# Performance work log

Measured on AMD Instinct MI355X. Metric: run time of the kernel, lower is better.

Reference implementation:

```python
import jax, jax.numpy as jnp
import numpy as np

V_WORD, V_ENT, V_REL = 50000, 200000, 1000
B, S, CTX, T = 64, 128, 256, 10
E, D, H, C = 300, 100, 256, 3  # input_dim, triples_embedding_dim, hidden, classes
IN = E + 2 * D  # LSTM input size in graph_attention mode


def setup_inputs() -> dict:
    key = jax.random.key(0)
    ks = jax.random.split(key, 16)
    inputs = jax.random.randint(ks[0], (B, S), 0, V_WORD)
    context = jax.random.randint(ks[1], (B, CTX), 0, V_WORD)
    triples = jax.random.randint(ks[2], (B, S, T, 3), 0, V_REL)
    lengths = jax.random.randint(ks[3], (B,), 1, S + 1)  # valid lengths >= 1
    # id2_ids_batch: -1 sentinel means "no triple"; mix of -1 and valid
    id2_ids_batch = jax.random.randint(ks[4], (B, S, T), 0, 2) * 2 - 1
    embedding = jax.random.normal(ks[5], (V_WORD, E), jnp.float32) * 0.02
    embeddings_entity = jax.random.normal(ks[6], (V_ENT, D), jnp.float32) * 0.02
    embeddings_relation = jax.random.normal(ks[7], (V_REL, D), jnp.float32) * 0.02
    W_ent = jax.random.normal(ks[8], (D, 2 * D), jnp.float32) * 0.05  # entity_transformed (no bias)
    W_ih = jax.random.normal(ks[9], (4 * H, IN), jnp.float32) * 0.05
    W_hh = jax.random.normal(ks[10], (4 * H, H), jnp.float32) * 0.05
    b_lstm = jnp.zeros((4 * H,), jnp.float32)
    attn_w = jax.random.normal(ks[11], (1, H), jnp.float32) * 0.05
    attn_b = jnp.zeros((1,), jnp.float32)
    out_w = jax.random.normal(ks[12], (C, H), jnp.float32) * 0.05
    out_b = jnp.zeros((C,), jnp.float32)
    return dict(inputs=inputs, context=context, triples=triples, lengths=lengths,
                id2_ids_batch=id2_ids_batch, embedding=embedding,
                embeddings_entity=embeddings_entity, embeddings_relation=embeddings_relation,
                W_ent=W_ent, W_ih=W_ih, W_hh=W_hh, b_lstm=b_lstm,
                attn_w=attn_w, attn_b=attn_b, out_w=out_w, out_b=out_b)


def _lstm(x, W_ih, W_hh, b):
    """Single-layer unidirectional LSTM, PyTorch gate order (i,f,g,o). x: [B,S,I] -> [B,S,H]."""
    Hh = W_hh.shape[1]
    xg = jnp.einsum('bsi,gi->bsg', x, W_ih) + b  # precompute input projections [B,S,4H]
    def step(carry, xg_t):
        h, c = carry
        g = xg_t + h @ W_hh.T
        i, f, gg, o = jnp.split(g, 4, axis=-1)
        c = jax.nn.sigmoid(f) * c + jax.nn.sigmoid(i) * jnp.tanh(gg)
        h = jax.nn.sigmoid(o) * jnp.tanh(c)
        return (h, c), h
    h0 = jnp.zeros((x.shape[0], Hh), x.dtype)
    _, hs = jax.lax.scan(step, (h0, h0), jnp.swapaxes(xg, 0, 1))
    return jnp.swapaxes(hs, 0, 1)


def reference(inputs, context, triples, lengths, id2_ids_batch, embedding,
              embeddings_entity, embeddings_relation, W_ent, W_ih, W_hh, b_lstm,
              attn_w, attn_b, out_w, out_b):
    x = embedding[inputs]  # [B,S,E]
    # graph_attention branch, vectorized over (batch, token, triple)
    eh = embeddings_entity[triples[..., 0]]   # [B,S,T,D]
    et = embeddings_entity[triples[..., 1]]   # [B,S,T,D]
    er = embeddings_relation[triples[..., 2]] # [B,S,T,D]
    ht = jnp.concatenate([eh, et], axis=-1)   # [B,S,T,2D]
    tr = jnp.tanh(jnp.einsum('bstk,dk->bstd', ht, W_ent))  # entity_transformed + tanh
    e = jnp.sum(tr * er, axis=-1)             # [B,S,T]
    alpha = jax.nn.softmax(e, axis=-1)        # softmax over triples
    graph = jnp.einsum('bst,bstk->bsk', alpha, ht)  # [B,S,2D]
    valid = jnp.any(id2_ids_batch != -1, axis=-1)   # [B,S]; all -1 -> zeros (cc branch)
    graph = jnp.where(valid[..., None], graph, 0.0)
    t_in = jnp.concatenate([x, graph], axis=-1)     # [B,S,E+2D]
    out = _lstm(t_in, W_ih, W_hh, b_lstm)           # [B,S,H]
    # 'att' attention pooling, masked by lengths (pack/pad equivalent)
    mask = jnp.arange(S)[None, :] < lengths[:, None]
    scores = (jnp.einsum('bsh,oh->bso', out, attn_w) + attn_b)[..., 0]  # [B,S]
    a = jax.nn.softmax(jnp.where(mask, scores, -1e9), axis=-1)
    attended = jnp.einsum('bs,bsh->bh', a, out)     # [B,H]
    logits = attended @ out_w.T + out_b             # [B,C]
    return logits
```

## Files before the change

kernel.cpp:

```cpp
#include <hip/hip_runtime.h>
#include <cstdint>
#include <cstddef>

typedef unsigned int  uint_t;
typedef unsigned short ushort_t;

constexpr int B_  = 64;
constexpr int S_  = 128;
constexpr int D_  = 100;
constexpr int E_  = 300;
constexpr int H_  = 256;
constexpr int KIN = 512;
constexpr int NG  = 1024;
constexpr int M_  = B_ * S_;

constexpr size_t OFF_WT   = 0;
constexpr size_t OFF_FLAG = 40000;
constexpr size_t OFF_WIH  = 40960;
constexpr size_t OFF_WHH  = OFF_WIH + (size_t)NG * KIN * 2;
constexpr size_t OFF_TIN  = OFF_WHH + (size_t)128 * NG * 4;
constexpr size_t OFF_XG   = OFF_TIN + (size_t)M_ * KIN * 2;
constexpr size_t OFF_HOUT = OFF_XG + (size_t)M_ * NG * 4;

__device__ __forceinline__ float b2f(ushort_t u) {
  union { uint_t u; float f; } v; v.u = ((uint_t)u) << 16; return v.f;
}
__device__ __forceinline__ float blo(uint_t u) {
  union { uint_t u; float f; } v; v.u = u << 16; return v.f;
}
__device__ __forceinline__ float bhi(uint_t u) {
  union { uint_t u; float f; } v; v.u = u & 0xffff0000u; return v.f;
}
__device__ __forceinline__ ushort_t f2b(float f) {
  union { float f; uint_t u; } v; v.f = f;
  uint_t r = (v.u + 0x7fffu + ((v.u >> 16) & 1u)) >> 16;
  return (ushort_t)r;
}
__device__ __forceinline__ ushort_t f16bits(float f) {
  _Float16 h = (_Float16)f;
  union { _Float16 h; ushort_t u; } v; v.h = h; return v.u;
}
__device__ __forceinline__ uint_t pk16(float a, float b) {
  return (uint_t)f16bits(a) | ((uint_t)f16bits(b) << 16);
}
__device__ __forceinline__ float fast_tanh(float x) {
  float e = __expf(2.f * x);
  return 1.f - 2.f / (e + 1.f);
}
__device__ __forceinline__ float sigm(float x) {
  return 1.f / (1.f + __expf(-x));
}
__device__ __forceinline__ float ldv(const void* p, size_t i, int f32) {
  return f32 ? ((const float*)p)[i] : b2f(((const ushort_t*)p)[i]);
}

__device__ __forceinline__ float dot2(uint_t w, uint_t h, float acc) {
  union { uint_t u; _Float16 h[2]; } a, b; a.u = w; b.u = h;
  acc += (float)a.h[0] * (float)b.h[0];
  acc += (float)a.h[1] * (float)b.h[1];
  return acc;
}

__global__ __launch_bounds__(64) void k_detect(const uint_t* __restrict__ emb_w,
                                               char* __restrict__ ws)
{
  int tid = threadIdx.x;
  int hits = 0;
  for (int i = 0; i < 8; ++i) {
    uint_t w = emb_w[i * 64 + tid];
    uint_t e = (w >> 7) & 0xffu;
    hits += (e >= 140) ? 1 : 0;
  }
  for (int off = 32; off > 0; off >>= 1) hits += __shfl_down(hits, off);
  if (tid == 0) *(int*)(ws + OFF_FLAG) = (hits >= 32) ? 1 : 0;
}

__global__ __launch_bounds__(256) void k0_prep(
    const void* __restrict__ W_ent, const void* __restrict__ W_ih,
    const void* __restrict__ W_hh, char* __restrict__ ws)
{
  const int f32 = *(const int*)(ws + OFF_FLAG);
  int id = blockIdx.x * 256 + threadIdx.x;
  uint_t*   Wt = (uint_t*)(ws + OFF_WT);
  ushort_t* Wp = (ushort_t*)(ws + OFF_WIH);
  uint_t*   W2 = (uint_t*)(ws + OFF_WHH);
  if (id < 10000) {
    int kp = id / 100, d = id % 100;
    float a = ldv(W_ent, (size_t)d * 200 + 2 * kp,     f32);
    float b = ldv(W_ent, (size_t)d * 200 + 2 * kp + 1, f32);
    Wt[id] = pk16(a, b);
  } else if (id >= 20000 && id < 20000 + NG * KIN) {
    int i = id - 20000;
    int n = i >> 9, k = i & 511;
    Wp[i] = (k < 500) ? f2b(ldv(W_ih, (size_t)n * 500 + k, f32)) : (ushort_t)0;
  } else if (id >= 20000 + NG * KIN && id < 20000 + NG * KIN + 128 * NG) {
    int i = id - 20000 - NG * KIN;
    int row = i >> 7, kp = i & 127;
    float a = ldv(W_hh, (size_t)row * 256 + 2 * kp,     f32);
    float b = ldv(W_hh, (size_t)row * 256 + 2 * kp + 1, f32);
    W2[i] = pk16(a, b);
  }
}

__global__ __launch_bounds__(512) void k1_graph(
    const int* __restrict__ inputs, const int* __restrict__ triples,
    const int* __restrict__ id2, const void* __restrict__ emb,
    const void* __restrict__ ent, const void* __restrict__ rel,
    char* __restrict__ ws)
{
  __shared__ __align__(16) uint_t Wl2[10000];
  __shared__ uint_t htp[4][10][100];
  __shared__ float er_l[4][10][100];
  __shared__ float e_l[4][10];
  __shared__ float alpha_l[4][10];
  __shared__ int   trip_l[4][30];
  __shared__ int   vflag[4];

  const int tid = threadIdx.x;
  const int j   = tid >> 7;
  const int lt  = tid & 127;
  const int m   = blockIdx.x * 4 + j;
  const int f32 = *(const int*)(ws + OFF_FLAG);
  ushort_t* tin = (ushort_t*)(ws + OFF_TIN);

  if (lt < 30) trip_l[j][lt] = triples[(size_t)m * 30 + lt];
  if (lt == 0) vflag[j] = 0;
  if (lt < 10) e_l[j][lt] = 0.f;
  __syncthreads();
  if (lt < 10 && id2[(size_t)m * 10 + lt] != -1) atomicOr(&vflag[j], 1);

  {
    const uint4* src = (const uint4*)(ws + OFF_WT);
    uint4* dst = (uint4*)Wl2;
    for (int i = tid; i < 2500; i += 512) dst[i] = src[i];
  }
  for (int i = lt; i < 1000; i += 128) {
    int t = i / 100, kp = i % 100;
    int row = trip_l[j][t * 3 + (kp < 50 ? 0 : 1)];
    int off = (kp < 50) ? 2 * kp : 2 * (kp - 50);
    float x0, x1;
    if (f32) {
      float2 v = *(const float2*)((const float*)ent + (size_t)row * 100 + off);
      x0 = v.x; x1 = v.y;
    } else {
      uint_t u = *(const uint_t*)((const ushort_t*)ent + (size_t)row * 100 + off);
      x0 = blo(u); x1 = bhi(u);
    }
    htp[j][t][kp] = pk16(x0, x1);
  }
  for (int i = lt; i < 1000; i += 128) {
    int t = i / 100, d = i % 100;
    er_l[j][t][d] = ldv(rel, (size_t)trip_l[j][t * 3 + 2] * 100 + d, f32);
  }
  {
    int w = inputs[m];
    for (int c = lt; c < 300; c += 128)
      tin[(size_t)m * KIN + c] = f2b(ldv(emb, (size_t)w * E_ + c, f32));
    if (lt < 12) tin[(size_t)m * KIN + 500 + lt] = 0;
  }
  __syncthreads();

  if (lt < 125) {
    int t2 = lt / 25, d4 = lt % 25;
    int t0 = 2 * t2, t1 = t0 + 1;
    const uint_t* h0p = htp[j][t0];
    const uint_t* h1p = htp[j][t1];
    float a00 = 0, a01 = 0, a02 = 0, a03 = 0;
    float a10 = 0, a11 = 0, a12 = 0, a13 = 0;
    for (int kp = 0; kp < 100; ++kp) {
      uint4 wv = *(const uint4*)&Wl2[kp * 100 + 4 * d4];
      uint_t hp0 = h0p[kp], hp1 = h1p[kp];
      a00 = dot2(wv.x, hp0, a00); a01 = dot2(wv.y, hp0, a01);
      a02 = dot2(wv.z, hp0, a02); a03 = dot2(wv.w, hp0, a03);
      a10 = dot2(wv.x, hp1, a10); a11 = dot2(wv.y, hp1, a11);
      a12 = dot2(wv.z, hp1, a12); a13 = dot2(wv.w, hp1, a13);
    }
    int d = 4 * d4;
    float s0 = fast_tanh(a00) * er_l[j][t0][d]     + fast_tanh(a01) * er_l[j][t0][d + 1]
             + fast_tanh(a02) * er_l[j][t0][d + 2] + fast_tanh(a03) * er_l[j][t0][d + 3];
    float s1 = fast_tanh(a10) * er_l[j][t1][d]     + fast_tanh(a11) * er_l[j][t1][d + 1]
             + fast_tanh(a12) * er_l[j][t1][d + 2] + fast_tanh(a13) * er_l[j][t1][d + 3];
    atomicAdd(&e_l[j][t0], s0);
    atomicAdd(&e_l[j][t1], s1);
  }
  __syncthreads();
  if (lt == 0) {
    float mx = e_l[j][0];
    for (int t = 1; t < 10; ++t) mx = fmaxf(mx, e_l[j][t]);
    float s = 0.f;
    for (int t = 0; t < 10; ++t) { float v = __expf(e_l[j][t] - mx); alpha_l[j][t] = v; s += v; }
    float inv = 1.f / s;
    for (int t = 0; t < 10; ++t) alpha_l[j][t] *= inv;
  }
  __syncthreads();
  for (int kp = lt; kp < 100; kp += 128) {
    float g0 = 0.f, g1 = 0.f;
#pragma unroll
    for (int t = 0; t < 10; ++t) {
      union { uint_t u; _Float16 h[2]; } v; v.u = htp[j][t][kp];
      g0 += alpha_l[j][t] * (float)v.h[0];
      g1 += alpha_l[j][t] * (float)v.h[1];
    }
    if (!vflag[j]) { g0 = 0.f; g1 = 0.f; }
    tin[(size_t)m * KIN + 300 + 2 * kp]     = f2b(g0);
    tin[(size_t)m * KIN + 300 + 2 * kp + 1] = f2b(g1);
  }
}

typedef __attribute__((ext_vector_type(8))) short short8;
typedef __attribute__((ext_vector_type(4))) float f32x4;
typedef _Float16 half8 __attribute__((ext_vector_type(8)));

__global__ __launch_bounds__(256) void k2_xg(
    const void* __restrict__ bl, char* __restrict__ ws)
{
  __shared__ __align__(16) ushort_t As[128 * 32];
  __shared__ __align__(16) ushort_t Bs[128 * 32];
  const ushort_t* A  = (const ushort_t*)(ws + OFF_TIN);
  const ushort_t* Bw = (const ushort_t*)(ws + OFF_WIH);
  float* xg = (float*)(ws + OFF_XG);
  const int f32 = *(const int*)(ws + OFF_FLAG);

  const int tid = threadIdx.x;
  const int m0 = blockIdx.x * 128;
  const int n0 = blockIdx.y * 128;
  const int lane = tid & 63, wv = tid >> 6;
  const int wm = wv & 1, wn = wv >> 1;
  const int g = lane >> 4, r = lane & 15;

  f32x4 acc[4][4] = {};

  for (int ks = 0; ks < 16; ++ks) {
    const int k0 = ks * 32;
    {
      int c0 = tid, c1 = tid + 256;
      uint4 a0 = *(const uint4*)(A  + (size_t)(m0 + (c0 >> 2)) * KIN + k0 + ((c0 & 3) << 3));
      uint4 a1 = *(const uint4*)(A  + (size_t)(m0 + (c1 >> 2)) * KIN + k0 + ((c1 & 3) << 3));
      uint4 b0 = *(const uint4*)(Bw + (size_t)(n0 + (c0 >> 2)) * KIN + k0 + ((c0 & 3) << 3));
      uint4 b1 = *(const uint4*)(Bw + (size_t)(n0 + (c1 >> 2)) * KIN + k0 + ((c1 & 3) << 3));
      ((uint4*)As)[c0] = a0; ((uint4*)As)[c1] = a1;
      ((uint4*)Bs)[c0] = b0; ((uint4*)Bs)[c1] = b1;
    }
    __syncthreads();
    short8 av[4], bv[4];
#pragma unroll
    for (int i = 0; i < 4; ++i)
      av[i] = *(const short8*)&As[(wm * 64 + i * 16 + r) * 32 + g * 8];
#pragma unroll
    for (int j = 0; j < 4; ++j)
      bv[j] = *(const short8*)&Bs[(wn * 64 + j * 16 + r) * 32 + g * 8];
#pragma unroll
    for (int i = 0; i < 4; ++i)
#pragma unroll
      for (int j = 0; j < 4; ++j)
        acc[i][j] = __builtin_amdgcn_mfma_f32_16x16x32_bf16(av[i], bv[j], acc[i][j], 0, 0, 0);
    __syncthreads();
  }
#pragma unroll
  for (int j = 0; j < 4; ++j) {
    int n = n0 + wn * 64 + j * 16 + r;
    float bias = ldv(bl, n, f32);
#pragma unroll
    for (int i = 0; i < 4; ++i) {
      int mrow = m0 + wm * 64 + i * 16 + g * 4;
#pragma unroll
      for (int rr = 0; rr < 4; ++rr)
        xg[(size_t)(mrow + rr) * NG + n] = acc[i][j][rr] + bias;
    }
  }
}

__global__ __attribute__((amdgpu_waves_per_eu(2, 2))) __launch_bounds__(512)
void k3_lstm(char* __restrict__ ws)
{
  extern __shared__ __align__(16) char smem[];
  uint4*    ldsw = (uint4*)smem;
  float*    gbuf = (float*)(smem + 16 * 512 * 16);
  ushort_t* hbuf = (ushort_t*)(smem + 16 * 512 * 16 + 4096);

  const int tid = threadIdx.x;
  const int b   = blockIdx.x;
  const int w   = tid >> 6;
  const int l   = tid & 63;
  const int r   = l & 15;
  const int g   = l >> 4;
  const int rowbase = w * 128;

  const uint_t* W2 = (const uint_t*)(ws + OFF_WHH);
  const float* xg = (const float*)(ws + OFF_XG);
  float* hout = (float*)(ws + OFF_HOUT);

  uint4 wfrag[6][8];
#pragma unroll
  for (int mt = 0; mt < 6; ++mt)
#pragma unroll
    for (int kt = 0; kt < 8; ++kt)
      wfrag[mt][kt] = *(const uint4*)&W2[(size_t)(rowbase + mt * 16 + r) * 128 + kt * 16 + g * 4];
#pragma unroll
  for (int mt = 6; mt < 8; ++mt)
#pragma unroll
    for (int kt = 0; kt < 8; ++kt)
      ldsw[((mt - 6) * 8 + kt) * 512 + tid] =
        *(const uint4*)&W2[(size_t)(rowbase + mt * 16 + r) * 128 + kt * 16 + g * 4];

  hbuf[tid] = 0;
  float c = 0.f;
  const int bm = b * S_;
  float xn0 = 0.f, xn1 = 0.f, xn2 = 0.f, xn3 = 0.f;
  if (tid < 256) {
    const float* xp = xg + (size_t)bm * NG;
    xn0 = xp[tid]; xn1 = xp[tid + 256]; xn2 = xp[tid + 512]; xn3 = xp[tid + 768];
  }
  __syncthreads();

  for (int t = 0; t < S_; ++t) {
    const int cur = t & 1;
    const uint_t* hb = (const uint_t*)(hbuf + cur * 256);
#pragma unroll
    for (int hf = 0; hf < 2; ++hf) {
      f32x4 acc[4] = {};
#pragma unroll
      for (int kt = 0; kt < 8; ++kt) {
        union { uint4 u; half8 h; } bf;
        bf.u = make_uint4(0, 0, 0, 0);
        if (r == 0) bf.u = *(const uint4*)&hb[kt * 16 + g * 4];
#pragma unroll
        for (int m4 = 0; m4 < 4; ++m4) {
          const int mt = hf * 4 + m4;
          union { uint4 u; half8 h; } af;
          if (mt < 6) af.u = wfrag[mt][kt];
          else        af.u = ldsw[((mt - 6) * 8 + kt) * 512 + tid];
          acc[m4] = __builtin_amdgcn_mfma_f32_16x16x32_f16(af.h, bf.h, acc[m4], 0, 0, 0);
        }
      }
      if (r == 0) {
#pragma unroll
        for (int m4 = 0; m4 < 4; ++m4) {
          const int row = rowbase + (hf * 4 + m4) * 16 + g * 4;
          gbuf[row + 0] = acc[m4][0];
          gbuf[row + 1] = acc[m4][1];
          gbuf[row + 2] = acc[m4][2];
          gbuf[row + 3] = acc[m4][3];
        }
      }
    }
    __syncthreads();
    if (tid < 256) {
      float gi = gbuf[tid]       + xn0;
      float gf = gbuf[tid + 256] + xn1;
      float gg = gbuf[tid + 512] + xn2;
      float go = gbuf[tid + 768] + xn3;
      if (t + 1 < S_) {
        const float* xq = xg + (size_t)(bm + t + 1) * NG;
        xn0 = xq[tid]; xn1 = xq[tid + 256]; xn2 = xq[tid + 512]; xn3 = xq[tid + 768];
      }
      c = sigm(gf) * c + sigm(gi) * fast_tanh(gg);
      float hv = sigm(go) * fast_tanh(c);
      hout[(size_t)(bm + t) * H_ + tid] = hv;
      hbuf[(cur ^ 1) * 256 + tid] = f16bits(hv);
    }
    __syncthreads();
  }
}

__global__ __launch_bounds__(256) void k4_attn(
    const int* __restrict__ lengths, const void* __restrict__ attn_w,
    const void* __restrict__ attn_b, const void* __restrict__ out_w,
    const void* __restrict__ out_b, const char* __restrict__ ws,
    void* __restrict__ out)
{
  __shared__ float aw[256];
  __shared__ float sc[128];
  __shared__ float at[256];
  __shared__ float red[256];

  const int tid = threadIdx.x;
  const int b = blockIdx.x;
  const int f32 = *(const int*)(ws + OFF_FLAG);
  const float* hout = (const float*)(ws + OFF_HOUT);
  const int bm = b * S_;

  aw[tid] = ldv(attn_w, tid, f32);
  __syncthreads();
  if (tid < 128) {
    const float* hp = hout + (size_t)(bm + tid) * H_;
    float acc = 0.f;
    for (int k = 0; k < 256; k += 4) {
      float4 h4 = *(const float4*)(hp + k);
      acc += h4.x * aw[k] + h4.y * aw[k + 1] + h4.z * aw[k + 2] + h4.w * aw[k + 3];
    }
    sc[tid] = acc + ldv(attn_b, 0, f32);
  }
  __syncthreads();
  if (tid == 0) {
    int len = lengths[b];
    float mx = -3.4e38f;
    for (int s = 0; s < len; ++s) mx = fmaxf(mx, sc[s]);
    float sum = 0.f;
    for (int s = 0; s < 128; ++s) {
      float v = (s < len) ? __expf(sc[s] - mx) : 0.f;
      sc[s] = v; sum += v;
    }
    float inv = 1.f / sum;
    for (int s = 0; s < 128; ++s) sc[s] *= inv;
  }
  __syncthreads();
  {
    float acc = 0.f;
    for (int s = 0; s < 128; ++s)
      acc += sc[s] * hout[(size_t)(bm + s) * H_ + tid];
    at[tid] = acc;
  }
  __syncthreads();
  for (int cc = 0; cc < 3; ++cc) {
    red[tid] = at[tid] * ldv(out_w, cc * 256 + tid, f32);
    __syncthreads();
    for (int off = 128; off > 0; off >>= 1) {
      if (tid < off) red[tid] += red[tid + off];
      __syncthreads();
    }
    if (tid == 0) {
      float v = red[0] + ldv(out_b, cc, f32);
      if (f32) ((float*)out)[b * 3 + cc] = v;
      else     ((ushort_t*)out)[b * 3 + cc] = f2b(v);
    }
    __syncthreads();
  }
}

extern "C" void kernel_launch(void* const* d_in, const int* in_sizes, int n_in,
                              void* d_out, int out_size, void* d_ws, size_t ws_size,
                              hipStream_t stream)
{
  const int* inputs  = (const int*)d_in[0];
  const int* triples = (const int*)d_in[2];
  const int* lengths = (const int*)d_in[3];
  const int* id2     = (const int*)d_in[4];
  const void* emb    = d_in[5];
  const void* ent    = d_in[6];
  const void* rel    = d_in[7];
  const void* W_ent  = d_in[8];
  const void* W_ih   = d_in[9];
  const void* W_hh   = d_in[10];
  const void* b_lstm = d_in[11];
  const void* attn_w = d_in[12];
  const void* attn_b = d_in[13];
  const void* out_w  = d_in[14];
  const void* out_b  = d_in[15];
  char* ws = (char*)d_ws;

  constexpr int K3_SMEM = 16 * 512 * 16 + 4096 + 2 * 256 * 2;
  static bool attr_set = false;
  if (!attr_set) {
    (void)hipFuncSetAttribute((const void*)k3_lstm,
                              hipFuncAttributeMaxDynamicSharedMemorySize, K3_SMEM);
    attr_set = true;
  }

  k_detect<<<dim3(1), dim3(64), 0, stream>>>((const uint_t*)emb, ws);
  k0_prep<<<dim3(2639), dim3(256), 0, stream>>>(W_ent, W_ih, W_hh, ws);
  k1_graph<<<dim3(M_ / 4), dim3(512), 0, stream>>>(inputs, triples, id2, emb, ent, rel, ws);
  k2_xg<<<dim3(64, 8), dim3(256), 0, stream>>>(b_lstm, ws);
  k3_lstm<<<dim3(B_), dim3(512), K3_SMEM, stream>>>(ws);
  k4_attn<<<dim3(B_), dim3(256), 0, stream>>>(lengths, attn_w, attn_b, out_w, out_b, ws, d_out);
}
```

Baseline: 591.6 us.

## Batch 16 sequences per LSTM block using full MFMA N dimension

```diff
diff --git a/kernel.cpp b/kernel.cpp
--- a/kernel.cpp
+++ b/kernel.cpp
@@ -95,10 +95,12 @@
     Wp[i] = (k < 500) ? f2b(ldv(W_ih, (size_t)n * 500 + k, f32)) : (ushort_t)0;
   } else if (id >= 20000 + NG * KIN && id < 20000 + NG * KIN + 128 * NG) {
     int i = id - 20000 - NG * KIN;
-    int row = i >> 7, kp = i & 127;
-    float a = ldv(W_hh, (size_t)row * 256 + 2 * kp,     f32);
-    float b = ldv(W_hh, (size_t)row * 256 + 2 * kp + 1, f32);
-    W2[i] = pk16(a, b);
+    int p = i >> 7, kp = i & 127;
+    int u = p >> 2, gate = p & 3;
+    int orig = u + gate * 256;
+    float a = ldv(W_hh, (size_t)orig * 256 + 2 * kp,     f32);
+    float b = ldv(W_hh, (size_t)orig * 256 + 2 * kp + 1, f32);
+    W2[(size_t)p * 128 + kp] = pk16(a, b);
   }
 }
 
@@ -260,12 +262,13 @@
   for (int j = 0; j < 4; ++j) {
     int n = n0 + wn * 64 + j * 16 + r;
     float bias = ldv(bl, n, f32);
+    int np = 4 * (n & 255) + (n >> 8);
 #pragma unroll
     for (int i = 0; i < 4; ++i) {
       int mrow = m0 + wm * 64 + i * 16 + g * 4;
 #pragma unroll
       for (int rr = 0; rr < 4; ++rr)
-        xg[(size_t)(mrow + rr) * NG + n] = acc[i][j][rr] + bias;
+        xg[(size_t)(mrow + rr) * NG + np] = acc[i][j][rr] + bias;
     }
   }
 }
@@ -275,17 +278,18 @@
 {
   extern __shared__ __align__(16) char smem[];
   uint4*    ldsw = (uint4*)smem;
-  float*    gbuf = (float*)(smem + 16 * 512 * 16);
-  ushort_t* hbuf = (ushort_t*)(smem + 16 * 512 * 16 + 4096);
+  ushort_t* hbuf = (ushort_t*)(smem + 16 * 512 * 16);
 
   const int tid = threadIdx.x;
-  const int b   = blockIdx.x;
   const int w   = tid >> 6;
   const int l   = tid & 63;
   const int r   = l & 15;
   const int g   = l >> 4;
   const int rowbase = w * 128;
 
+  const int batch = blockIdx.x * 16 + r;
+  const int bm = batch * S_;
+
   const uint_t* W2 = (const uint_t*)(ws + OFF_WHH);
   const float* xg = (const float*)(ws + OFF_XG);
   float* hout = (float*)(ws + OFF_HOUT);
@@ -303,61 +307,44 @@
       ldsw[((mt - 6) * 8 + kt) * 512 + tid] =
         *(const uint4*)&W2[(size_t)(rowbase + mt * 16 + r) * 128 + kt * 16 + g * 4];
 
-  hbuf[tid] = 0;
-  float c = 0.f;
-  const int bm = b * S_;
-  float xn0 = 0.f, xn1 = 0.f, xn2 = 0.f, xn3 = 0.f;
-  if (tid < 256) {
-    const float* xp = xg + (size_t)bm * NG;
-    xn0 = xp[tid]; xn1 = xp[tid + 256]; xn2 = xp[tid + 512]; xn3 = xp[tid + 768];
-  }
+  for (int i = tid; i < 2 * 16 * 264; i += 512) hbuf[i] = 0;
+  float cst[8] = {0.f, 0.f, 0.f, 0.f, 0.f, 0.f, 0.f, 0.f};
   __syncthreads();
 
   for (int t = 0; t < S_; ++t) {
-    const int cur = t & 1;
-    const uint_t* hb = (const uint_t*)(hbuf + cur * 256);
-#pragma unroll
-    for (int hf = 0; hf < 2; ++hf) {
-      f32x4 acc[4] = {};
-#pragma unroll
-      for (int kt = 0; kt < 8; ++kt) {
-        union { uint4 u; half8 h; } bf;
-        bf.u = make_uint4(0, 0, 0, 0);
-        if (r == 0) bf.u = *(const uint4*)&hb[kt * 16 + g * 4];
-#pragma unroll
-        for (int m4 = 0; m4 < 4; ++m4) {
-          const int mt = hf * 4 + m4;
-          union { uint4 u; half8 h; } af;
-          if (mt < 6) af.u = wfrag[mt][kt];
-          else        af.u = ldsw[((mt - 6) * 8 + kt) * 512 + tid];
-          acc[m4] = __builtin_amdgcn_mfma_f32_16x16x32_f16(af.h, bf.h, acc[m4], 0, 0, 0);
-        }
+    const ushort_t* hb = hbuf + (t & 1) * (16 * 264);
+    ushort_t*       hw = hbuf + ((t & 1) ^ 1) * (16 * 264);
+    f32x4 acc[8] = {};
+#pragma unroll
+    for (int kt = 0; kt < 8; ++kt) {
+      union { uint4 u; half8 h; } bf;
+      bf.u = *(const uint4*)&hb[r * 264 + kt * 32 + g * 8];
+#pragma unroll
+      for (int mt = 0; mt < 6; ++mt) {
+        union { uint4 u; half8 h; } af; af.u = wfrag[mt][kt];
+        acc[mt] = __builtin_amdgcn_mfma_f32_16x16x32_f16(af.h, bf.h, acc[mt], 0, 0, 0);
       }
-      if (r == 0) {
-#pragma unroll
-        for (int m4 = 0; m4 < 4; ++m4) {
-          const int row = rowbase + (hf * 4 + m4) * 16 + g * 4;
-          gbuf[row + 0] = acc[m4][0];
-          gbuf[row + 1] = acc[m4][1];
-          gbuf[row + 2] = acc[m4][2];
-          gbuf[row + 3] = acc[m4][3];
-        }
+      {
+        union { uint4 u; half8 h; } a6; a6.u = ldsw[(0 * 8 + kt) * 512 + tid];
+        acc[6] = __builtin_amdgcn_mfma_f32_16x16x32_f16(a6.h, bf.h, acc[6], 0, 0, 0);
+        union { uint4 u; half8 h; } a7; a7.u = ldsw[(1 * 8 + kt) * 512 + tid];
+        acc[7] = __builtin_amdgcn_mfma_f32_16x16x32_f16(a7.h, bf.h, acc[7], 0, 0, 0);
       }
     }
-    __syncthreads();
-    if (tid < 256) {
-      float gi = gbuf[tid]       + xn0;
-      float gf = gbuf[tid + 256] + xn1;
-      float gg = gbuf[tid + 512] + xn2;
-      float go = gbuf[tid + 768] + xn3;
-      if (t + 1 < S_) {
-        const float* xq = xg + (size_t)(bm + t + 1) * NG;
-        xn0 = xq[tid]; xn1 = xq[tid + 256]; xn2 = xq[tid + 512]; xn3 = xq[tid + 768];
-      }
-      c = sigm(gf) * c + sigm(gi) * fast_tanh(gg);
-      float hv = sigm(go) * fast_tanh(c);
-      hout[(size_t)(bm + t) * H_ + tid] = hv;
-      hbuf[(cur ^ 1) * 256 + tid] = f16bits(hv);
+    const float* xrow = xg + (size_t)(bm + t) * NG;
+    float* horow = hout + (size_t)(bm + t) * H_;
+#pragma unroll
+    for (int mt = 0; mt < 8; ++mt) {
+      const int u = w * 32 + mt * 4 + g;
+      float4 x4 = *(const float4*)&xrow[4 * u];
+      float gi = acc[mt][0] + x4.x;
+      float gf = acc[mt][1] + x4.y;
+      float gg = acc[mt][2] + x4.z;
+      float go = acc[mt][3] + x4.w;
+      cst[mt] = sigm(gf) * cst[mt] + sigm(gi) * fast_tanh(gg);
+      float hv = sigm(go) * fast_tanh(cst[mt]);
+      horow[u] = hv;
+      hw[r * 264 + u] = f16bits(hv);
     }
     __syncthreads();
   }
@@ -449,7 +436,7 @@
   const void* out_b  = d_in[15];
   char* ws = (char*)d_ws;
 
-  constexpr int K3_SMEM = 16 * 512 * 16 + 4096 + 2 * 256 * 2;
+  constexpr int K3_SMEM = 16 * 512 * 16 + 2 * 16 * 264 * 2;
   static bool attr_set = false;
   if (!attr_set) {
     (void)hipFuncSetAttribute((const void*)k3_lstm,
@@ -461,6 +448,6 @@
   k0_prep<<<dim3(2639), dim3(256), 0, stream>>>(W_ent, W_ih, W_hh, ws);
   k1_graph<<<dim3(M_ / 4), dim3(512), 0, stream>>>(inputs, triples, id2, emb, ent, rel, ws);
   k2_xg<<<dim3(64, 8), dim3(256), 0, stream>>>(b_lstm, ws);
-  k3_lstm<<<dim3(B_), dim3(512), K3_SMEM, stream>>>(ws);
+  k3_lstm<<<dim3(B_ / 16), dim3(512), K3_SMEM, stream>>>(ws);
   k4_attn<<<dim3(B_), dim3(256), 0, stream>>>(lengths, attn_w, attn_b, out_w, out_b, ws, d_out);
 }
```

Result: slower. 1.219 ms (+106.0%).
